# Optimization experiments

Hardware: AMD Instinct MI355X
Metric: run time of the kernel (lower is better)

The kernel has to match this reference:

```python
import jax, jax.numpy as jnp
import numpy as np

N_SAMPLES = 64
N_AGENTS = 64          # agents per sample (fully connected subgraph)
N = N_SAMPLES * N_AGENTS
F_DIM = 128            # decoder_latent_size
EDIM = 2
ZDIM = 2 * F_DIM + EDIM
BN_EPS = 1e-5


def _build_edge_index():
    # fully-connected (no self loops) per sample, with node offsets, COO row-major
    idx = np.arange(N_AGENTS)
    rows = np.repeat(idx, N_AGENTS)
    cols = np.tile(idx, N_AGENTS)
    mask = rows != cols
    rows, cols = rows[mask], cols[mask]
    offs = (np.arange(N_SAMPLES) * N_AGENTS)[:, None]
    src = (rows[None, :] + offs).ravel().astype(np.int32)  # edge_index[0] = source j
    dst = (cols[None, :] + offs).ravel().astype(np.int32)  # edge_index[1] = target i
    return src, dst


def setup_inputs() -> dict:
    key = jax.random.key(0)
    ks = jax.random.split(key, 12)
    src, dst = _build_edge_index()
    s = 1.0 / np.sqrt(ZDIM)
    inp = {
        "gnn_in": jax.random.normal(ks[0], (N, F_DIM), dtype=jnp.float32),
        "centers": jax.random.normal(ks[1], (N, EDIM), dtype=jnp.float32),
        "src": jnp.asarray(src),
        "dst": jnp.asarray(dst),
        "Wf1": jax.random.normal(ks[2], (F_DIM, ZDIM), dtype=jnp.float32) * s,
        "bf1": jnp.zeros((F_DIM,), jnp.float32),
        "Ws1": jax.random.normal(ks[3], (F_DIM, ZDIM), dtype=jnp.float32) * s,
        "bs1": jnp.zeros((F_DIM,), jnp.float32),
        "g1": jnp.ones((F_DIM,), jnp.float32),
        "be1": jnp.zeros((F_DIM,), jnp.float32),
        "Wf2": jax.random.normal(ks[4], (F_DIM, ZDIM), dtype=jnp.float32) * s,
        "bf2": jnp.zeros((F_DIM,), jnp.float32),
        "Ws2": jax.random.normal(ks[5], (F_DIM, ZDIM), dtype=jnp.float32) * s,
        "bs2": jnp.zeros((F_DIM,), jnp.float32),
        "g2": jnp.ones((F_DIM,), jnp.float32),
        "be2": jnp.zeros((F_DIM,), jnp.float32),
    }
    return inp


def _cgconv(x, edge_attr, src, dst, Wf, bf, Ws, bs, gamma, beta):
    # z_ij = [x_i, x_j, e_ij]  (i = target = dst, j = source = src)
    z = jnp.concatenate([x[dst], x[src], edge_attr], axis=-1)        # [E, 2F+2]
    msg = jax.nn.sigmoid(z @ Wf.T + bf) * jax.nn.softplus(z @ Ws.T + bs)  # [E, F]
    agg = jax.ops.segment_sum(msg, dst, num_segments=N)              # [N, F]
    # BatchNorm1d (training mode: batch stats, biased var), then residual
    mean = agg.mean(axis=0)
    var = agg.var(axis=0)
    agg = (agg - mean) * jax.lax.rsqrt(var + BN_EPS) * gamma + beta
    return agg + x


def reference(gnn_in, centers, src, dst,
              Wf1, bf1, Ws1, bs1, g1, be1,
              Wf2, bf2, Ws2, bs2, g2, be2):
    edge_attr = centers[dst] - centers[src]                           # data[cols] - data[rows]
    x = jax.nn.relu(_cgconv(gnn_in, edge_attr, src, dst, Wf1, bf1, Ws1, bs1, g1, be1))
    out = jax.nn.relu(_cgconv(x, edge_attr, src, dst, Wf2, bf2, Ws2, bs2, g2, be2))
    # original splits per sample; uniform sample size -> concatenation == out itself
    return out
```

## Files before the change

kernel.cpp:

```cpp
#include <hip/hip_runtime.h>

constexpr int NS = 64;
constexpr int NA = 64;
constexpr int NN = NS * NA;
constexpr int FD = 128;
constexpr int ZD = 2 * FD + 2;
constexpr int FS = 16;
constexpr int NB = NS * (FD / FS);
constexpr int NT = 512;
constexpr int XPAD = 132;
constexpr float BN_EPS = 1e-5f;
constexpr float L2E = 1.44269504088896f;
constexpr float LN2 = 0.69314718055995f;

__global__ __launch_bounds__(256) void pack_kernel(
    const float* __restrict__ Wf1, const float* __restrict__ Ws1, float4* __restrict__ WT1,
    const float* __restrict__ Wf2, const float* __restrict__ Ws2, float4* __restrict__ WT2,
    float* __restrict__ stats)
{
    int gidx = blockIdx.x * 256 + threadIdx.x;
    if (gidx < 512) stats[gidx] = 0.0f;
    const float* Wf; const float* Ws; float4* WT; int i;
    if (gidx < FD * FD) { Wf = Wf1; Ws = Ws1; WT = WT1; i = gidx; }
    else                { Wf = Wf2; Ws = Ws2; WT = WT2; i = gidx - FD * FD; }
    int k = i >> 7, f = i & 127;
    WT[i] = make_float4(Wf[f * ZD + k], Wf[f * ZD + FD + k],
                        Ws[f * ZD + k], Ws[f * ZD + FD + k]);
}

__device__ __forceinline__ void layer_body(
    const float (*xs)[XPAD], const float2* cs, float2 (*q)[FS],
    const float4* __restrict__ WT4,
    const float* __restrict__ Wf, const float* __restrict__ Ws,
    const float* __restrict__ bf, const float* __restrict__ bs,
    int tid, int fl, int ig, int f, int base,
    float* __restrict__ agg, float* __restrict__ S, float* __restrict__ SS)
{
    float aPf0=0.f,aQf0=0.f,aPs0=0.f,aQs0=0.f;
    float aPf1=0.f,aQf1=0.f,aPs1=0.f,aQs1=0.f;
    const float4* Wp = WT4 + f;
    #pragma unroll 4
    for (int k = 0; k < FD; ++k) {
        float4 w = Wp[k * FD];
        float x0 = xs[ig][k];
        float x1 = xs[ig + 32][k];
        aPf0 = fmaf(x0, w.x, aPf0); aQf0 = fmaf(x0, w.y, aQf0);
        aPs0 = fmaf(x0, w.z, aPs0); aQs0 = fmaf(x0, w.w, aQs0);
        aPf1 = fmaf(x1, w.x, aPf1); aQf1 = fmaf(x1, w.y, aQf1);
        aPs1 = fmaf(x1, w.z, aPs1); aQs1 = fmaf(x1, w.w, aQs1);
    }
    float we0 = Wf[f*ZD + 2*FD], we1 = Wf[f*ZD + 2*FD + 1];
    float ws0 = Ws[f*ZD + 2*FD], ws1 = Ws[f*ZD + 2*FD + 1];
    float bfv = bf[f], bsv = bs[f];
    float2 c0 = cs[ig], c1 = cs[ig + 32];
    float cf0 = c0.x*we0 + c0.y*we1, cg0 = c0.x*ws0 + c0.y*ws1;
    float cf1 = c1.x*we0 + c1.y*we1, cg1 = c1.x*ws0 + c1.y*ws1;
    float Pf0 = aPf0 + cf0 + bfv, Ps0 = aPs0 + cg0 + bsv;
    float Pf1 = aPf1 + cf1 + bfv, Ps1 = aPs1 + cg1 + bsv;
    float Qf0 = aQf0 - cf0,       Qs0 = aQs0 - cg0;
    float Qf1 = aQf1 - cf1,       Qs1 = aQs1 - cg1;
    float2 p0 = make_float2(__builtin_amdgcn_exp2f(-Pf0*L2E), __builtin_amdgcn_exp2f(Ps0*L2E));
    float2 p1 = make_float2(__builtin_amdgcn_exp2f(-Pf1*L2E), __builtin_amdgcn_exp2f(Ps1*L2E));
    q[ig][fl]    = make_float2(__builtin_amdgcn_exp2f(-Qf0*L2E), __builtin_amdgcn_exp2f(Qs0*L2E));
    q[ig+32][fl] = make_float2(__builtin_amdgcn_exp2f(-Qf1*L2E), __builtin_amdgcn_exp2f(Qs1*L2E));
    __syncthreads();

    float a0=0.f, a1=0.f, b0=0.f, b1=0.f;
    #pragma unroll 4
    for (int j = 0; j < NA; j += 2) {
        float2 qa = q[j][fl];
        float2 qb = q[j+1][fl];
        a0 = fmaf(__builtin_amdgcn_rcpf(1.0f + p0.x*qa.x),
                  __builtin_amdgcn_logf(1.0f + p0.y*qa.y), a0);
        b0 = fmaf(__builtin_amdgcn_rcpf(1.0f + p1.x*qa.x),
                  __builtin_amdgcn_logf(1.0f + p1.y*qa.y), b0);
        a1 = fmaf(__builtin_amdgcn_rcpf(1.0f + p0.x*qb.x),
                  __builtin_amdgcn_logf(1.0f + p0.y*qb.y), a1);
        b1 = fmaf(__builtin_amdgcn_rcpf(1.0f + p1.x*qb.x),
                  __builtin_amdgcn_logf(1.0f + p1.y*qb.y), b1);
    }
    float aA = a0 + a1, aB = b0 + b1;
    {
        float2 qv0 = q[ig][fl];
        aA -= __builtin_amdgcn_rcpf(1.0f + p0.x*qv0.x) *
              __builtin_amdgcn_logf(1.0f + p0.y*qv0.y);
        float2 qv1 = q[ig+32][fl];
        aB -= __builtin_amdgcn_rcpf(1.0f + p1.x*qv1.x) *
              __builtin_amdgcn_logf(1.0f + p1.y*qv1.y);
    }
    aA *= LN2; aB *= LN2;
    agg[(base + ig) * FD + f]      = aA;
    agg[(base + ig + 32) * FD + f] = aB;

    __syncthreads();
    float* sm = (float*)q;
    sm[tid]      = aA + aB;
    sm[NT + tid] = aA*aA + aB*aB;
    __syncthreads();
    if (tid < FS) {
        float sv = 0.f, qv = 0.f;
        #pragma unroll
        for (int r = 0; r < 32; ++r) {
            sv += sm[r * FS + tid];
            qv += sm[NT + r * FS + tid];
        }
        atomicAdd(&S[(f - fl) + tid], sv);
        atomicAdd(&SS[(f - fl) + tid], qv);
    }
}

__global__ __launch_bounds__(NT) void layer1_kernel(
    const float* __restrict__ X0, const float* __restrict__ C,
    const float4* __restrict__ WT4,
    const float* __restrict__ Wf, const float* __restrict__ Ws,
    const float* __restrict__ bf, const float* __restrict__ bs,
    float* __restrict__ agg, float* __restrict__ S, float* __restrict__ SS)
{
    __shared__ float xs[NA][XPAD];
    __shared__ float2 q[NA][FS];
    __shared__ float2 cs[NA];
    int tid = threadIdx.x, bid = blockIdx.x;
    int s = bid & (NS - 1), fq = bid >> 6;
    int base = s * NA;
    const float4* Xv = (const float4*)(X0 + base * FD);
    for (int idx = tid; idx < NA * FD / 4; idx += NT) {
        int n = idx >> 5, k4 = idx & 31;
        *(float4*)&xs[n][k4 * 4] = Xv[idx];
    }
    if (tid < NA) cs[tid] = ((const float2*)C)[base + tid];
    __syncthreads();
    layer_body(xs, cs, q, WT4, Wf, Ws, bf, bs,
               tid, tid & 15, tid >> 4, fq * FS + (tid & 15), base, agg, S, SS);
}

__global__ __launch_bounds__(NT) void layer2_kernel(
    const float* __restrict__ X0, const float* __restrict__ agg1,
    const float* __restrict__ C,
    const float* __restrict__ S1, const float* __restrict__ SS1,
    const float* __restrict__ g1, const float* __restrict__ be1,
    const float4* __restrict__ WT4,
    const float* __restrict__ Wf, const float* __restrict__ Ws,
    const float* __restrict__ bf, const float* __restrict__ bs,
    float* __restrict__ agg2, float* __restrict__ S2, float* __restrict__ SS2)
{
    __shared__ float xs[NA][XPAD];
    __shared__ float2 q[NA][FS];
    __shared__ float2 cs[NA];
    __shared__ float bnsc[FD], bnsh[FD];
    int tid = threadIdx.x, bid = blockIdx.x;
    int s = bid & (NS - 1), fq = bid >> 6;
    int base = s * NA;
    if (tid < FD) {
        float m  = S1[tid] * (1.0f / NN);
        float v  = SS1[tid] * (1.0f / NN) - m * m;
        float sc = g1[tid] * rsqrtf(v + BN_EPS);
        bnsc[tid] = sc;
        bnsh[tid] = be1[tid] - m * sc;
    }
    if (tid < NA) cs[tid] = ((const float2*)C)[base + tid];
    __syncthreads();
    const float4* Xv = (const float4*)(X0 + base * FD);
    const float4* Av = (const float4*)(agg1 + base * FD);
    for (int idx = tid; idx < NA * FD / 4; idx += NT) {
        int n = idx >> 5, k4 = (idx & 31) * 4;
        float4 x = Xv[idx], a = Av[idx];
        xs[n][k4 + 0] = fmaxf(fmaf(a.x, bnsc[k4 + 0], bnsh[k4 + 0]) + x.x, 0.0f);
        xs[n][k4 + 1] = fmaxf(fmaf(a.y, bnsc[k4 + 1], bnsh[k4 + 1]) + x.y, 0.0f);
        xs[n][k4 + 2] = fmaxf(fmaf(a.z, bnsc[k4 + 2], bnsh[k4 + 2]) + x.z, 0.0f);
        xs[n][k4 + 3] = fmaxf(fmaf(a.w, bnsc[k4 + 3], bnsh[k4 + 3]) + x.w, 0.0f);
    }
    __syncthreads();
    layer_body(xs, cs, q, WT4, Wf, Ws, bf, bs,
               tid, tid & 15, tid >> 4, fq * FS + (tid & 15), base, agg2, S2, SS2);
}

__global__ __launch_bounds__(256) void out_kernel(
    const float4* __restrict__ X0, const float4* __restrict__ A1,
    const float4* __restrict__ A2,
    const float* __restrict__ S1, const float* __restrict__ SS1,
    const float* __restrict__ g1, const float* __restrict__ be1,
    const float* __restrict__ S2, const float* __restrict__ SS2,
    const float* __restrict__ g2, const float* __restrict__ be2,
    float4* __restrict__ out)
{
    int idx = blockIdx.x * 256 + threadIdx.x;
    int f0 = (idx & 31) * 4;
    float4 x = X0[idx], a1 = A1[idx], a2 = A2[idx];
    float r[4], xv[4] = {x.x, x.y, x.z, x.w};
    float a1v[4] = {a1.x, a1.y, a1.z, a1.w}, a2v[4] = {a2.x, a2.y, a2.z, a2.w};
    #pragma unroll
    for (int j = 0; j < 4; ++j) {
        int f = f0 + j;
        float m1  = S1[f] * (1.0f / NN);
        float v1  = SS1[f] * (1.0f / NN) - m1 * m1;
        float sc1 = g1[f] * rsqrtf(v1 + BN_EPS);
        float sh1 = be1[f] - m1 * sc1;
        float x1  = fmaxf(fmaf(a1v[j], sc1, sh1) + xv[j], 0.0f);
        float m2  = S2[f] * (1.0f / NN);
        float v2  = SS2[f] * (1.0f / NN) - m2 * m2;
        float sc2 = g2[f] * rsqrtf(v2 + BN_EPS);
        float sh2 = be2[f] - m2 * sc2;
        r[j] = fmaxf(fmaf(a2v[j], sc2, sh2) + x1, 0.0f);
    }
    out[idx] = make_float4(r[0], r[1], r[2], r[3]);
}

extern "C" void kernel_launch(void* const* d_in, const int* in_sizes, int n_in,
                              void* d_out, int out_size, void* d_ws, size_t ws_size,
                              hipStream_t stream) {
    const float* gnn_in  = (const float*)d_in[0];
    const float* centers = (const float*)d_in[1];
    const float* Wf1 = (const float*)d_in[4];
    const float* bf1 = (const float*)d_in[5];
    const float* Ws1 = (const float*)d_in[6];
    const float* bs1 = (const float*)d_in[7];
    const float* g1  = (const float*)d_in[8];
    const float* be1 = (const float*)d_in[9];
    const float* Wf2 = (const float*)d_in[10];
    const float* bf2 = (const float*)d_in[11];
    const float* Ws2 = (const float*)d_in[12];
    const float* bs2 = (const float*)d_in[13];
    const float* g2  = (const float*)d_in[14];
    const float* be2 = (const float*)d_in[15];

    char* ws = (char*)d_ws;
    float4* WT1   = (float4*)(ws);
    float4* WT2   = (float4*)(ws + (256 << 10));
    float*  agg1  = (float*) (ws + (512 << 10));
    float*  agg2  = (float*) (ws + (512 << 10) + (2 << 20));
    float*  stats = (float*) (ws + (512 << 10) + (4 << 20));
    float *S1 = stats, *SS1 = stats + 128, *S2 = stats + 256, *SS2 = stats + 384;

    pack_kernel<<<128, 256, 0, stream>>>(Wf1, Ws1, WT1, Wf2, Ws2, WT2, stats);
    layer1_kernel<<<NB, NT, 0, stream>>>(gnn_in, centers, WT1,
                                         Wf1, Ws1, bf1, bs1, agg1, S1, SS1);
    layer2_kernel<<<NB, NT, 0, stream>>>(gnn_in, agg1, centers, S1, SS1, g1, be1,
                                         WT2, Wf2, Ws2, bf2, bs2, agg2, S2, SS2);
    out_kernel<<<NN * FD / 1024, 256, 0, stream>>>(
        (const float4*)gnn_in, (const float4*)agg1, (const float4*)agg2,
        S1, SS1, g1, be1, S2, SS2, g2, be2, (float4*)d_out);
}
```

Measured before the change: 139.5 us.

## Stage weights in LDS per block, drop pack kernel and atomics

Removes the separate weight-packing kernel; each block instead gathers its 16-feature weight slice from the raw Wf/Ws matrices into shared memory and reads it from LDS in the inner loop. BatchNorm statistics are written as per-sample partial sums instead of global atomics, which also removes the need to zero the stats buffer, and consumers reduce the 64 partials. Layer 2 stores the post-ReLU x1, so the output kernel only applies the second normalization. The cost is extra strided global reads for the weight gather in every block, 32 KB more LDS per block (which may lower occupancy), and an extra x1 write.

```diff
diff --git a/kernel.cpp b/kernel.cpp
--- a/kernel.cpp
+++ b/kernel.cpp
@@ -13,35 +13,36 @@
 constexpr float L2E = 1.44269504088896f;
 constexpr float LN2 = 0.69314718055995f;
 
-__global__ __launch_bounds__(256) void pack_kernel(
-    const float* __restrict__ Wf1, const float* __restrict__ Ws1, float4* __restrict__ WT1,
-    const float* __restrict__ Wf2, const float* __restrict__ Ws2, float4* __restrict__ WT2,
-    float* __restrict__ stats)
-{
-    int gidx = blockIdx.x * 256 + threadIdx.x;
-    if (gidx < 512) stats[gidx] = 0.0f;
-    const float* Wf; const float* Ws; float4* WT; int i;
-    if (gidx < FD * FD) { Wf = Wf1; Ws = Ws1; WT = WT1; i = gidx; }
-    else                { Wf = Wf2; Ws = Ws2; WT = WT2; i = gidx - FD * FD; }
-    int k = i >> 7, f = i & 127;
-    WT[i] = make_float4(Wf[f * ZD + k], Wf[f * ZD + FD + k],
-                        Ws[f * ZD + k], Ws[f * ZD + FD + k]);
+__device__ __forceinline__ void stage_w(
+    float4 (*wlds)[FS], const float* __restrict__ Wf, const float* __restrict__ Ws,
+    int fq, int t0, int tstep)
+{
+    for (int i = t0; i < FD * FS; i += tstep) {
+        int k = i >> 4, fr = i & (FS - 1);
+        int row = (fq * FS + fr) * ZD;
+        wlds[k][fr] = make_float4(Wf[row + k], Wf[row + FD + k],
+                                  Ws[row + k], Ws[row + FD + k]);
+    }
 }
 
 __device__ __forceinline__ void layer_body(
     const float (*xs)[XPAD], const float2* cs, float2 (*q)[FS],
-    const float4* __restrict__ WT4,
+    const float4 (*wlds)[FS],
     const float* __restrict__ Wf, const float* __restrict__ Ws,
     const float* __restrict__ bf, const float* __restrict__ bs,
-    int tid, int fl, int ig, int f, int base,
-    float* __restrict__ agg, float* __restrict__ S, float* __restrict__ SS)
-{
+    int tid, int s, int fq,
+    float* __restrict__ agg, float* __restrict__ pS, float* __restrict__ pSS)
+{
+    const int fl = tid & (FS - 1);
+    const int ig = tid >> 4;
+    const int f  = fq * FS + fl;
+    const int base = s * NA;
+
     float aPf0=0.f,aQf0=0.f,aPs0=0.f,aQs0=0.f;
     float aPf1=0.f,aQf1=0.f,aPs1=0.f,aQs1=0.f;
-    const float4* Wp = WT4 + f;
     #pragma unroll 4
     for (int k = 0; k < FD; ++k) {
-        float4 w = Wp[k * FD];
+        float4 w = wlds[k][fl];
         float x0 = xs[ig][k];
         float x1 = xs[ig + 32][k];
         aPf0 = fmaf(x0, w.x, aPf0); aQf0 = fmaf(x0, w.y, aQf0);
@@ -104,24 +105,25 @@
             sv += sm[r * FS + tid];
             qv += sm[NT + r * FS + tid];
         }
-        atomicAdd(&S[(f - fl) + tid], sv);
-        atomicAdd(&SS[(f - fl) + tid], qv);
+        pS [s * FD + fq * FS + tid] = sv;
+        pSS[s * FD + fq * FS + tid] = qv;
     }
 }
 
 __global__ __launch_bounds__(NT) void layer1_kernel(
     const float* __restrict__ X0, const float* __restrict__ C,
-    const float4* __restrict__ WT4,
     const float* __restrict__ Wf, const float* __restrict__ Ws,
     const float* __restrict__ bf, const float* __restrict__ bs,
-    float* __restrict__ agg, float* __restrict__ S, float* __restrict__ SS)
+    float* __restrict__ agg, float* __restrict__ pS, float* __restrict__ pSS)
 {
     __shared__ float xs[NA][XPAD];
     __shared__ float2 q[NA][FS];
+    __shared__ float4 wlds[FD][FS];
     __shared__ float2 cs[NA];
     int tid = threadIdx.x, bid = blockIdx.x;
     int s = bid & (NS - 1), fq = bid >> 6;
     int base = s * NA;
+    stage_w(wlds, Wf, Ws, fq, tid, NT);
     const float4* Xv = (const float4*)(X0 + base * FD);
     for (int idx = tid; idx < NA * FD / 4; idx += NT) {
         int n = idx >> 5, k4 = idx & 31;
@@ -129,80 +131,93 @@
     }
     if (tid < NA) cs[tid] = ((const float2*)C)[base + tid];
     __syncthreads();
-    layer_body(xs, cs, q, WT4, Wf, Ws, bf, bs,
-               tid, tid & 15, tid >> 4, fq * FS + (tid & 15), base, agg, S, SS);
+    layer_body(xs, cs, q, wlds, Wf, Ws, bf, bs, tid, s, fq, agg, pS, pSS);
 }
 
 __global__ __launch_bounds__(NT) void layer2_kernel(
     const float* __restrict__ X0, const float* __restrict__ agg1,
     const float* __restrict__ C,
-    const float* __restrict__ S1, const float* __restrict__ SS1,
+    const float* __restrict__ pS1, const float* __restrict__ pSS1,
     const float* __restrict__ g1, const float* __restrict__ be1,
-    const float4* __restrict__ WT4,
     const float* __restrict__ Wf, const float* __restrict__ Ws,
     const float* __restrict__ bf, const float* __restrict__ bs,
-    float* __restrict__ agg2, float* __restrict__ S2, float* __restrict__ SS2)
+    float* __restrict__ x1, float* __restrict__ agg2,
+    float* __restrict__ pS2, float* __restrict__ pSS2)
 {
     __shared__ float xs[NA][XPAD];
     __shared__ float2 q[NA][FS];
+    __shared__ float4 wlds[FD][FS];
     __shared__ float2 cs[NA];
     __shared__ float bnsc[FD], bnsh[FD];
     int tid = threadIdx.x, bid = blockIdx.x;
     int s = bid & (NS - 1), fq = bid >> 6;
     int base = s * NA;
     if (tid < FD) {
-        float m  = S1[tid] * (1.0f / NN);
-        float v  = SS1[tid] * (1.0f / NN) - m * m;
+        float sv = 0.f, qv = 0.f;
+        #pragma unroll
+        for (int s2 = 0; s2 < NS; ++s2) {
+            sv += pS1[s2 * FD + tid];
+            qv += pSS1[s2 * FD + tid];
+        }
+        float m  = sv * (1.0f / NN);
+        float v  = qv * (1.0f / NN) - m * m;
         float sc = g1[tid] * rsqrtf(v + BN_EPS);
         bnsc[tid] = sc;
         bnsh[tid] = be1[tid] - m * sc;
-    }
-    if (tid < NA) cs[tid] = ((const float2*)C)[base + tid];
-    __syncthreads();
-    const float4* Xv = (const float4*)(X0 + base * FD);
-    const float4* Av = (const float4*)(agg1 + base * FD);
+    } else {
+        stage_w(wlds, Wf, Ws, fq, tid - FD, NT - FD);
+        if (tid >= NT - NA) cs[tid - (NT - NA)] = ((const float2*)C)[base + tid - (NT - NA)];
+    }
+    __syncthreads();
+    const float4* Xv  = (const float4*)(X0 + base * FD);
+    const float4* Av  = (const float4*)(agg1 + base * FD);
+    float4*       X1v = (float4*)(x1 + base * FD);
     for (int idx = tid; idx < NA * FD / 4; idx += NT) {
         int n = idx >> 5, k4 = (idx & 31) * 4;
         float4 x = Xv[idx], a = Av[idx];
-        xs[n][k4 + 0] = fmaxf(fmaf(a.x, bnsc[k4 + 0], bnsh[k4 + 0]) + x.x, 0.0f);
-        xs[n][k4 + 1] = fmaxf(fmaf(a.y, bnsc[k4 + 1], bnsh[k4 + 1]) + x.y, 0.0f);
-        xs[n][k4 + 2] = fmaxf(fmaf(a.z, bnsc[k4 + 2], bnsh[k4 + 2]) + x.z, 0.0f);
-        xs[n][k4 + 3] = fmaxf(fmaf(a.w, bnsc[k4 + 3], bnsh[k4 + 3]) + x.w, 0.0f);
-    }
-    __syncthreads();
-    layer_body(xs, cs, q, WT4, Wf, Ws, bf, bs,
-               tid, tid & 15, tid >> 4, fq * FS + (tid & 15), base, agg2, S2, SS2);
-}
-
-__global__ __launch_bounds__(256) void out_kernel(
-    const float4* __restrict__ X0, const float4* __restrict__ A1,
-    const float4* __restrict__ A2,
-    const float* __restrict__ S1, const float* __restrict__ SS1,
-    const float* __restrict__ g1, const float* __restrict__ be1,
-    const float* __restrict__ S2, const float* __restrict__ SS2,
+        float4 r;
+        r.x = fmaxf(fmaf(a.x, bnsc[k4 + 0], bnsh[k4 + 0]) + x.x, 0.0f);
+        r.y = fmaxf(fmaf(a.y, bnsc[k4 + 1], bnsh[k4 + 1]) + x.y, 0.0f);
+        r.z = fmaxf(fmaf(a.z, bnsc[k4 + 2], bnsh[k4 + 2]) + x.z, 0.0f);
+        r.w = fmaxf(fmaf(a.w, bnsc[k4 + 3], bnsh[k4 + 3]) + x.w, 0.0f);
+        *(float4*)&xs[n][k4] = r;
+        X1v[idx] = r;
+    }
+    __syncthreads();
+    layer_body(xs, cs, q, wlds, Wf, Ws, bf, bs, tid, s, fq, agg2, pS2, pSS2);
+}
+
+__global__ __launch_bounds__(NT) void out_kernel(
+    const float4* __restrict__ x1, const float4* __restrict__ agg2,
+    const float* __restrict__ pS2, const float* __restrict__ pSS2,
     const float* __restrict__ g2, const float* __restrict__ be2,
     float4* __restrict__ out)
 {
-    int idx = blockIdx.x * 256 + threadIdx.x;
+    __shared__ float sc[FD], sh[FD];
+    int tid = threadIdx.x;
+    if (tid < FD) {
+        float sv = 0.f, qv = 0.f;
+        #pragma unroll
+        for (int s2 = 0; s2 < NS; ++s2) {
+            sv += pS2[s2 * FD + tid];
+            qv += pSS2[s2 * FD + tid];
+        }
+        float m  = sv * (1.0f / NN);
+        float v  = qv * (1.0f / NN) - m * m;
+        float scl = g2[tid] * rsqrtf(v + BN_EPS);
+        sc[tid] = scl;
+        sh[tid] = be2[tid] - m * scl;
+    }
+    __syncthreads();
+    int idx = blockIdx.x * NT + tid;
     int f0 = (idx & 31) * 4;
-    float4 x = X0[idx], a1 = A1[idx], a2 = A2[idx];
-    float r[4], xv[4] = {x.x, x.y, x.z, x.w};
-    float a1v[4] = {a1.x, a1.y, a1.z, a1.w}, a2v[4] = {a2.x, a2.y, a2.z, a2.w};
-    #pragma unroll
-    for (int j = 0; j < 4; ++j) {
-        int f = f0 + j;
-        float m1  = S1[f] * (1.0f / NN);
-        float v1  = SS1[f] * (1.0f / NN) - m1 * m1;
-        float sc1 = g1[f] * rsqrtf(v1 + BN_EPS);
-        float sh1 = be1[f] - m1 * sc1;
-        float x1  = fmaxf(fmaf(a1v[j], sc1, sh1) + xv[j], 0.0f);
-        float m2  = S2[f] * (1.0f / NN);
-        float v2  = SS2[f] * (1.0f / NN) - m2 * m2;
-        float sc2 = g2[f] * rsqrtf(v2 + BN_EPS);
-        float sh2 = be2[f] - m2 * sc2;
-        r[j] = fmaxf(fmaf(a2v[j], sc2, sh2) + x1, 0.0f);
-    }
-    out[idx] = make_float4(r[0], r[1], r[2], r[3]);
+    float4 xv = x1[idx], av = agg2[idx];
+    float4 r;
+    r.x = fmaxf(fmaf(av.x, sc[f0 + 0], sh[f0 + 0]) + xv.x, 0.0f);
+    r.y = fmaxf(fmaf(av.y, sc[f0 + 1], sh[f0 + 1]) + xv.y, 0.0f);
+    r.z = fmaxf(fmaf(av.z, sc[f0 + 2], sh[f0 + 2]) + xv.z, 0.0f);
+    r.w = fmaxf(fmaf(av.w, sc[f0 + 3], sh[f0 + 3]) + xv.w, 0.0f);
+    out[idx] = r;
 }
 
 extern "C" void kernel_launch(void* const* d_in, const int* in_sizes, int n_in,
@@ -224,19 +239,18 @@
     const float* be2 = (const float*)d_in[15];
 
     char* ws = (char*)d_ws;
-    float4* WT1   = (float4*)(ws);
-    float4* WT2   = (float4*)(ws + (256 << 10));
-    float*  agg1  = (float*) (ws + (512 << 10));
-    float*  agg2  = (float*) (ws + (512 << 10) + (2 << 20));
-    float*  stats = (float*) (ws + (512 << 10) + (4 << 20));
-    float *S1 = stats, *SS1 = stats + 128, *S2 = stats + 256, *SS2 = stats + 384;
-
-    pack_kernel<<<128, 256, 0, stream>>>(Wf1, Ws1, WT1, Wf2, Ws2, WT2, stats);
-    layer1_kernel<<<NB, NT, 0, stream>>>(gnn_in, centers, WT1,
-                                         Wf1, Ws1, bf1, bs1, agg1, S1, SS1);
-    layer2_kernel<<<NB, NT, 0, stream>>>(gnn_in, agg1, centers, S1, SS1, g1, be1,
-                                         WT2, Wf2, Ws2, bf2, bs2, agg2, S2, SS2);
-    out_kernel<<<NN * FD / 1024, 256, 0, stream>>>(
-        (const float4*)gnn_in, (const float4*)agg1, (const float4*)agg2,
-        S1, SS1, g1, be1, S2, SS2, g2, be2, (float4*)d_out);
-}
+    float* agg1  = (float*)(ws);
+    float* agg2  = (float*)(ws + (2 << 20));
+    float* x1    = (float*)(ws + (4 << 20));
+    float* p1S   = (float*)(ws + (6 << 20));
+    float* p1SS  = (float*)(ws + (6 << 20) + (32 << 10));
+    float* p2S   = (float*)(ws + (6 << 20) + (64 << 10));
+    float* p2SS  = (float*)(ws + (6 << 20) + (96 << 10));
+
+    layer1_kernel<<<NB, NT, 0, stream>>>(gnn_in, centers, Wf1, Ws1, bf1, bs1,
+                                         agg1, p1S, p1SS);
+    layer2_kernel<<<NB, NT, 0, stream>>>(gnn_in, agg1, centers, p1S, p1SS, g1, be1,
+                                         Wf2, Ws2, bf2, bs2, x1, agg2, p2S, p2SS);
+    out_kernel<<<NN * FD / 4 / NT, NT, 0, stream>>>(
+        (const float4*)x1, (const float4*)agg2, p2S, p2SS, g2, be2, (float4*)d_out);
+}
```

After: 130.9 us. 6.2% less time.
